# Optimization experiments

Hardware: AMD Instinct MI355X
Metric: run time of the kernel (lower is better)

Reference implementation:

```python
import jax, jax.numpy as jnp
import numpy as np

B, N, D, E = 256, 192, 512, 1024
H = E // 2          # MLP hidden = 512
K = 58              # round(0.3 * 192), hardcoded in the torch forward
EPS_L2 = 1e-8
EPS_BN = 1e-5


def setup_inputs() -> dict:
    key = jax.random.key(0)
    ks = jax.random.split(key, 8)
    s = 0.02
    return {
        "all_patch_embeddings": jax.random.normal(ks[0], (B, N, D), dtype=jnp.float32),
        "attention_map": jax.random.uniform(ks[1], (B, N + 1, N + 1), dtype=jnp.float32),
        # fc: Linear(D, E)
        "W_fc": jax.random.normal(ks[2], (E, D), dtype=jnp.float32) * s,
        "b_fc": jnp.zeros((E,), dtype=jnp.float32),
        # mlp layer 0: Linear(D, H) + BatchNorm1d(H) + ReLU
        "W1": jax.random.normal(ks[3], (H, D), dtype=jnp.float32) * s,
        "b1": jnp.zeros((H,), dtype=jnp.float32),
        "gamma1": jnp.ones((H,), dtype=jnp.float32),
        "beta1": jnp.zeros((H,), dtype=jnp.float32),
        # mlp layer 1: Linear(H, E) (no BN/ReLU applied on last layer)
        "W2": jax.random.normal(ks[4], (E, H), dtype=jnp.float32) * s,
        "b2": jnp.zeros((E,), dtype=jnp.float32),
    }


def reference(all_patch_embeddings, attention_map, W_fc, b_fc, W1, b1, gamma1, beta1, W2, b2):
    # CLS-row attention over the 192 patch tokens: [B, N]
    cls_attn = attention_map[:, 0, 1:]
    # torch.sort(descending)[...,:K] == top-k indices (batched, replaces python loop)
    _, idx = jax.lax.top_k(cls_attn, K)                      # [B, K] int32
    # batched gather replacing the per-sample index_select loop
    sel = jnp.take_along_axis(all_patch_embeddings, idx[:, :, None], axis=1)  # [B, K, D]
    # l2norm over last dim
    norm = jnp.sqrt(jnp.sum(sel * sel, axis=-1, keepdims=True)) + EPS_L2
    base = sel / norm
    # .half() cast in the original (round-trip to fp16 precision)
    base = base.astype(jnp.float16).astype(jnp.float32)
    # fc branch
    feat_fc = jnp.einsum('bkd,ed->bke', base, W_fc) + b_fc    # [B, K, E]
    # mlp branch (num_layers=2): Linear -> BN(train-mode batch stats) -> ReLU -> Linear
    h = jnp.einsum('bkd,hd->bkh', base, W1) + b1              # [B, K, H]
    hf = h.reshape(B * K, H)
    mu = jnp.mean(hf, axis=0)
    var = jnp.var(hf, axis=0)
    hf = (hf - mu) * jax.lax.rsqrt(var + EPS_BN) * gamma1 + beta1
    h = jax.nn.relu(hf).reshape(B, K, H)
    feat_mlp = jnp.einsum('bkh,eh->bke', h, W2) + b2          # [B, K, E]
    feats = feat_mlp + feat_fc
    # maxk_pool1d_var with k=1 and lengths == K reduces to max over token dim
    return jnp.max(feats, axis=1).astype(jnp.float32)         # [B, E]
```

## Files before the change

### kernel.cpp

```cpp
#include <hip/hip_runtime.h>
#include <hip/hip_fp16.h>

#define B_ 256
#define N_ 192
#define D_ 512
#define E_ 1024
#define H_ 512
#define K_ 58
#define M_ (B_*K_)
#define M2_ (B_*64)

typedef _Float16 f16;
typedef unsigned int u32;
typedef _Float16 half8 __attribute__((ext_vector_type(8)));
typedef float floatx16 __attribute__((ext_vector_type(16)));

#define WAIT_VMCNT0() asm volatile("s_waitcnt vmcnt(0)" ::: "memory")
#define BAR()         __builtin_amdgcn_s_barrier()
#define PRIO1()       __builtin_amdgcn_s_setprio(1)
#define PRIO0()       __builtin_amdgcn_s_setprio(0)

__device__ inline half8 cvt8(float4 f0, float4 f1) {
  half8 r;
  r[0]=(f16)f0.x; r[1]=(f16)f0.y; r[2]=(f16)f0.z; r[3]=(f16)f0.w;
  r[4]=(f16)f1.x; r[5]=(f16)f1.y; r[6]=(f16)f1.z; r[7]=(f16)f1.w;
  return r;
}

__device__ inline void gl_lds16(const f16* g, f16* l) {
  __builtin_amdgcn_global_load_lds((const __attribute__((address_space(1))) u32*)g,
                                   (__attribute__((address_space(3))) u32*)l, 16, 0, 0);
}

__device__ inline void stage128(const f16* gbase, int gstride, f16* sT, int w, int lane) {
  int lrow  = lane >> 2;
  int chunk = (lane & 3) ^ ((lane >> 3) & 3);
  gl_lds16(gbase + (size_t)(w*16      + lrow)*gstride + chunk*8, &sT[(w*16)*32]);
  gl_lds16(gbase + (size_t)(64 + w*16 + lrow)*gstride + chunk*8, &sT[(64 + w*16)*32]);
}

__device__ inline void stage_half(const f16* gbase, f16* sT, int h, int w, int lane) {
  int lrow = lane >> 3;
  int cg   = (lane & 7) ^ lrow;
  int r0 = h*128 + w*16;
  gl_lds16(gbase + (size_t)(r0     + lrow)*1024 + cg*8, &sT[(size_t)r0*64]);
  gl_lds16(gbase + (size_t)(r0 + 8 + lrow)*1024 + cg*8, &sT[(size_t)(r0 + 8)*64]);
}

__global__ void setup_kernel(const float* __restrict__ Wfc, const float* __restrict__ W2,
                             const float* __restrict__ W1, const float* __restrict__ attn,
                             const float* __restrict__ emb,
                             f16* __restrict__ Wcat, f16* __restrict__ W1_16,
                             f16* __restrict__ A16, float* __restrict__ csum) {
  __shared__ float sv[N_];
  __shared__ int sidx[K_];
  __shared__ int cnt;
  int blk = blockIdx.x, t = threadIdx.x;
  if (blk < 512) {
    int idx = (blk*256 + t)*8;
    int e = idx >> 10, c = idx & 1023;
    const float* src = (c < 512) ? (Wfc + (size_t)e*512 + c)
                                 : (W2  + (size_t)e*512 + (c-512));
    half8 o = cvt8(((const float4*)src)[0], ((const float4*)src)[1]);
    *(uint4*)(Wcat + idx) = *(uint4*)&o;
  } else if (blk < 640) {
    int idx = ((blk-512)*256 + t)*8;
    const float* src = W1 + idx;
    half8 o = cvt8(((const float4*)src)[0], ((const float4*)src)[1]);
    *(uint4*)(W1_16 + idx) = *(uint4*)&o;
  } else if (blk < 896) {
    int b = blk - 640;
    if (t == 0) cnt = 0;
    if (t < N_) sv[t] = attn[(size_t)b*193*193 + 1 + t];
    __syncthreads();
    if (t < N_) {
      float v = sv[t]; int rank = 0;
      for (int j = 0; j < N_; ++j) {
        float vj = sv[j];
        rank += (vj > v) || (vj == v && j < t);
      }
      if (rank < K_) sidx[atomicAdd(&cnt, 1)] = t;
    }
    __syncthreads();
    int w = t >> 6, lane = t & 63;
    for (int slot = w; slot < 64; slot += 4) {
      f16* dst = A16 + ((size_t)b*64 + slot)*1024 + lane*8;
      if (slot < K_) {
        const float* src = emb + ((size_t)b*N_ + sidx[slot])*D_ + lane*8;
        float4 v0 = ((const float4*)src)[0];
        float4 v1 = ((const float4*)src)[1];
        float s = v0.x*v0.x + v0.y*v0.y + v0.z*v0.z + v0.w*v0.w
                + v1.x*v1.x + v1.y*v1.y + v1.z*v1.z + v1.w*v1.w;
        #pragma unroll
        for (int off = 32; off > 0; off >>= 1) s += __shfl_xor(s, off);
        float inv = 1.0f / (sqrtf(s) + 1e-8f);
        half8 o;
        o[0]=(f16)(v0.x*inv); o[1]=(f16)(v0.y*inv); o[2]=(f16)(v0.z*inv); o[3]=(f16)(v0.w*inv);
        o[4]=(f16)(v1.x*inv); o[5]=(f16)(v1.y*inv); o[6]=(f16)(v1.z*inv); o[7]=(f16)(v1.w*inv);
        *(uint4*)dst = *(uint4*)&o;
      } else {
        uint4 z; z.x=0u; z.y=0u; z.z=0u; z.w=0u;
        *(uint4*)dst = z;
      }
    }
  } else {
    float4 z; z.x=0.f; z.y=0.f; z.z=0.f; z.w=0.f;
    ((float4*)csum)[t] = z;
  }
}

__launch_bounds__(256, 2)
__global__ void gemm1_kernel(const f16* __restrict__ A16, const f16* __restrict__ W1_16,
                             const float* __restrict__ b1, f16* __restrict__ Aout,
                             float* __restrict__ csum, float* __restrict__ css) {
  __shared__ f16 sA[2][128*32];
  __shared__ f16 sB[2][128*32];
  __shared__ float sSum[4][64], sSS[4][64];
  int t = threadIdx.x;
  int g = blockIdx.x;
  int xcd = g & 7, rest = g >> 3;
  int n0 = (rest & 3) * 128;
  int m0 = (xcd + 8*(rest >> 2)) * 128;
  int lane = t & 63, w = t >> 6;
  int l31 = lane & 31, khalf = lane >> 5, swz = (l31 >> 1) & 3;
  int rw = w & 1, cw = w >> 1;
  floatx16 acc[2][2] = {};
  const f16* Ab = A16 + (size_t)m0*1024;
  const f16* Bb = W1_16 + (size_t)n0*512;
  stage128(Ab, 1024, sA[0], w, lane);
  stage128(Bb, 512,  sB[0], w, lane);
  __syncthreads();
  for (int it = 0; it < 16; ++it) {
    int cur = it & 1, nxt = cur ^ 1;
    if (it < 15) {
      stage128(Ab + (it+1)*32, 1024, sA[nxt], w, lane);
      stage128(Bb + (it+1)*32, 512,  sB[nxt], w, lane);
    }
    #pragma unroll
    for (int s = 0; s < 2; ++s) {
      int ko = ((s*2 + khalf) ^ swz) * 8;
      half8 a[2], bf[2];
      #pragma unroll
      for (int i = 0; i < 2; ++i) a[i]  = *(const half8*)&sA[cur][(rw*64 + i*32 + l31)*32 + ko];
      #pragma unroll
      for (int j = 0; j < 2; ++j) bf[j] = *(const half8*)&sB[cur][(cw*64 + j*32 + l31)*32 + ko];
      #pragma unroll
      for (int i = 0; i < 2; ++i)
        #pragma unroll
        for (int j = 0; j < 2; ++j)
          acc[i][j] = __builtin_amdgcn_mfma_f32_32x32x16_f16(a[i], bf[j], acc[i][j], 0, 0, 0);
    }
    __syncthreads();
  }
  #pragma unroll
  for (int jt = 0; jt < 2; ++jt) {
    int col = n0 + cw*64 + jt*32 + l31;
    float bias = b1[col];
    float s = 0.f, ss = 0.f;
    #pragma unroll
    for (int i = 0; i < 2; ++i) {
      #pragma unroll
      for (int rg = 0; rg < 16; ++rg) {
        int rib = i*32 + (rg&3) + 8*(rg>>2) + 4*khalf;
        float x = acc[i][jt][rg] + bias;
        Aout[(size_t)(m0 + rw*64 + rib)*1024 + 512 + col] = (f16)x;
        if (i == 0 || rib < K_) { s += x; ss += x*x; }
      }
    }
    s  += __shfl_xor(s, 32);
    ss += __shfl_xor(ss, 32);
    if (lane < 32) { sSum[w][jt*32 + l31] = s; sSS[w][jt*32 + l31] = ss; }
  }
  __syncthreads();
  if (t < 128) {
    int c = t;
    int w0 = 2*(c >> 6), ci = c & 63;
    atomicAdd(&csum[n0 + c], sSum[w0][ci] + sSum[w0+1][ci]);
    atomicAdd(&css[n0 + c],  sSS[w0][ci]  + sSS[w0+1][ci]);
  }
}

__global__ void bnrelu_kernel(f16* __restrict__ A, const float* __restrict__ csum,
                              const float* __restrict__ css, const float* __restrict__ gamma,
                              const float* __restrict__ beta) {
  int t = threadIdx.x, lane = t & 63, w = t >> 6;
  int col = lane * 8;
  float sc[8], sh[8];
  #pragma unroll
  for (int j = 0; j < 8; ++j) {
    int c = col + j;
    float mu  = csum[c] * (1.0f/M_);
    float var = css[c] * (1.0f/M_) - mu*mu;
    float s   = gamma[c] * rsqrtf(var + 1e-5f);
    sc[j] = s; sh[j] = beta[c] - mu*s;
  }
  int r0 = blockIdx.x * 16 + w;
  #pragma unroll
  for (int i = 0; i < 4; ++i) {
    f16* p = A + (size_t)(r0 + i*4)*1024 + 512 + col;
    uint4 u = *(const uint4*)p;
    half8 v = *(half8*)&u, o;
    #pragma unroll
    for (int j = 0; j < 8; ++j) o[j] = (f16)fmaxf((float)v[j]*sc[j] + sh[j], 0.f);
    *(uint4*)p = *(uint4*)&o;
  }
}

__launch_bounds__(512, 2)
__global__ void fused_kernel(const f16* __restrict__ A16, const f16* __restrict__ Wcat,
                             const float* __restrict__ bfc, const float* __restrict__ b2,
                             float* __restrict__ out) {
  __shared__ __align__(16) f16 sA[2][256*64];
  __shared__ __align__(16) f16 sB[2][256*64];
  __shared__ float sMax[4][256];
  int t = threadIdx.x;
  int g = blockIdx.x;
  int xcd = g & 7, rest = g >> 3;
  int nt = rest & 3;
  int bt = xcd + 8*(rest >> 2);
  int e0 = nt * 256;
  int lane = t & 63, w = t >> 6;
  int l31 = lane & 31, khalf = lane >> 5, swzr = l31 & 7;
  int wm = w >> 2, wn = w & 3;
  floatx16 acc[4][2] = {};
  const f16* Ab = A16 + (size_t)bt*256*1024;
  const f16* Bb = Wcat + (size_t)e0*1024;
  int aBase0 = (wm*128 +  0 + l31)*64;
  int aBase1 = (wm*128 + 32 + l31)*64;
  int aBase2 = (wm*128 + 64 + l31)*64;
  int aBase3 = (wm*128 + 96 + l31)*64;
  int bBase0 = (wn*64  +  0 + l31)*64;
  int bBase1 = (wn*64  + 32 + l31)*64;
  stage_half(Ab, sA[0], 0, w, lane);
  stage_half(Ab, sA[0], 1, w, lane);
  stage_half(Bb, sB[0], 0, w, lane);
  stage_half(Bb, sB[0], 1, w, lane);
  WAIT_VMCNT0(); BAR();
  int cur = 0;
  #pragma unroll 1
  for (int it = 0; it < 16; ++it) {
    int nxt = cur ^ 1;
    const f16* An = Ab + (it+1)*64;
    const f16* Bn = Bb + (it+1)*64;
    const f16* sAc = sA[cur];
    const f16* sBc = sB[cur];
    half8 a0f[4], a1f[4], a2f[4], a3f[4], b0v[4], b1v[4];
    #pragma unroll
    for (int s = 0; s < 4; ++s) {
      int ko = (((s<<1)|khalf) ^ swzr) << 3;
      a0f[s] = *(const half8*)&sAc[aBase0 + ko];
      a1f[s] = *(const half8*)&sAc[aBase1 + ko];
      b0v[s] = *(const half8*)&sBc[bBase0 + ko];
    }
    if (it < 15) stage_half(An, sA[nxt], 0, w, lane);
    BAR(); PRIO1();
    #pragma unroll
    for (int s = 0; s < 4; ++s) {
      acc[0][0] = __builtin_amdgcn_mfma_f32_32x32x16_f16(a0f[s], b0v[s], acc[0][0], 0,0,0);
      acc[1][0] = __builtin_amdgcn_mfma_f32_32x32x16_f16(a1f[s], b0v[s], acc[1][0], 0,0,0);
    }
    PRIO0(); BAR();
    #pragma unroll
    for (int s = 0; s < 4; ++s) {
      int ko = (((s<<1)|khalf) ^ swzr) << 3;
      b1v[s] = *(const half8*)&sBc[bBase1 + ko];
    }
    if (it < 15) {
      stage_half(An, sA[nxt], 1, w, lane);
      stage_half(Bn, sB[nxt], 0, w, lane);
    }
    BAR(); PRIO1();
    #pragma unroll
    for (int s = 0; s < 4; ++s) {
      acc[0][1] = __builtin_amdgcn_mfma_f32_32x32x16_f16(a0f[s], b1v[s], acc[0][1], 0,0,0);
      acc[1][1] = __builtin_amdgcn_mfma_f32_32x32x16_f16(a1f[s], b1v[s], acc[1][1], 0,0,0);
    }
    PRIO0(); BAR();
    #pragma unroll
    for (int s = 0; s < 4; ++s) {
      int ko = (((s<<1)|khalf) ^ swzr) << 3;
      a2f[s] = *(const half8*)&sAc[aBase2 + ko];
      a3f[s] = *(const half8*)&sAc[aBase3 + ko];
    }
    if (it < 15) stage_half(Bn, sB[nxt], 1, w, lane);
    BAR(); PRIO1();
    #pragma unroll
    for (int s = 0; s < 4; ++s) {
      acc[2][1] = __builtin_amdgcn_mfma_f32_32x32x16_f16(a2f[s], b1v[s], acc[2][1], 0,0,0);
      acc[3][1] = __builtin_amdgcn_mfma_f32_32x32x16_f16(a3f[s], b1v[s], acc[3][1], 0,0,0);
    }
    PRIO0(); BAR();
    BAR(); PRIO1();
    #pragma unroll
    for (int s = 0; s < 4; ++s) {
      acc[2][0] = __builtin_amdgcn_mfma_f32_32x32x16_f16(a2f[s], b0v[s], acc[2][0], 0,0,0);
      acc[3][0] = __builtin_amdgcn_mfma_f32_32x32x16_f16(a3f[s], b0v[s], acc[3][0], 0,0,0);
    }
    PRIO0();
    WAIT_VMCNT0();
    BAR();
    cur = nxt;
  }
  #pragma unroll
  for (int p = 0; p < 2; ++p) {
    #pragma unroll
    for (int nf = 0; nf < 2; ++nf) {
      float mx = -3.0e38f;
      #pragma unroll
      for (int rg = 0; rg < 16; ++rg)
        mx = fmaxf(mx, acc[2*p][nf][rg]);
      #pragma unroll
      for (int rg = 0; rg < 16; ++rg) {
        int rowin = (rg&3) + 8*(rg>>2) + 4*khalf;
        if (rowin < K_ - 32) mx = fmaxf(mx, acc[2*p+1][nf][rg]);
      }
      mx = fmaxf(mx, __shfl_xor(mx, 32));
      if (lane < 32) sMax[wm*2 + p][wn*64 + nf*32 + l31] = mx;
    }
  }
  __syncthreads();
  #pragma unroll
  for (int j = 0; j < 2; ++j) {
    int idx = t + j*512;
    int bq = idx >> 8, c = idx & 255;
    int e = e0 + c;
    out[((size_t)bt*4 + bq)*E_ + e] = sMax[bq][c] + bfc[e] + b2[e];
  }
}

extern "C" void kernel_launch(void* const* d_in, const int* in_sizes, int n_in,
                              void* d_out, int out_size, void* d_ws, size_t ws_size,
                              hipStream_t stream) {
  const float* emb   = (const float*)d_in[0];
  const float* attn  = (const float*)d_in[1];
  const float* Wfc   = (const float*)d_in[2];
  const float* bfc   = (const float*)d_in[3];
  const float* W1    = (const float*)d_in[4];
  const float* b1    = (const float*)d_in[5];
  const float* gamma = (const float*)d_in[6];
  const float* beta  = (const float*)d_in[7];
  const float* W2    = (const float*)d_in[8];
  const float* b2    = (const float*)d_in[9];
  float* out = (float*)d_out;

  char* ws = (char*)d_ws;
  f16*   A16   = (f16*)(ws);
  f16*   Wcat  = (f16*)(ws + 33554432);
  f16*   W1_16 = (f16*)(ws + 35651584);
  float* csum  = (float*)(ws + 36175872);
  float* css   = (float*)(ws + 36177920);

  setup_kernel<<<897, 256, 0, stream>>>(Wfc, W2, W1, attn, emb, Wcat, W1_16, A16, csum);
  gemm1_kernel<<<512, 256, 0, stream>>>(A16, W1_16, b1, A16, csum, css);
  bnrelu_kernel<<<1024, 256, 0, stream>>>(A16, csum, css, gamma, beta);
  fused_kernel<<<256, 512, 0, stream>>>(A16, Wcat, bfc, b2, out);
}
```

Measured before the change: 235.2 us.

## Fuse BatchNorm+ReLU into final GEMM's A-tile staging, drop bnrelu kernel

Removes the separate bnrelu kernel. The fused GEMM now computes per-column scale and shift from the accumulated sums into shared memory. For the K-iterations covering the hidden half of A (iterations 7-14), it loads A through registers instead of global_load_lds, applies BN+ReLU, and writes the result into the swizzled LDS tile. This saves one kernel launch and a full read/write pass over the 16 MB hidden activation. In exchange, half of the A staging becomes synchronous register loads plus extra VALU work inside the main loop, which may reduce overlap.

```diff
diff --git a/kernel.cpp b/kernel.cpp
--- a/kernel.cpp
+++ b/kernel.cpp
@@ -16,6 +16,7 @@
 typedef float floatx16 __attribute__((ext_vector_type(16)));
 
 #define WAIT_VMCNT0() asm volatile("s_waitcnt vmcnt(0)" ::: "memory")
+#define WAIT_LGKM0()  asm volatile("s_waitcnt lgkmcnt(0)" ::: "memory")
 #define BAR()         __builtin_amdgcn_s_barrier()
 #define PRIO1()       __builtin_amdgcn_s_setprio(1)
 #define PRIO0()       __builtin_amdgcn_s_setprio(0)
@@ -25,6 +26,19 @@
   r[0]=(f16)f0.x; r[1]=(f16)f0.y; r[2]=(f16)f0.z; r[3]=(f16)f0.w;
   r[4]=(f16)f1.x; r[5]=(f16)f1.y; r[6]=(f16)f1.z; r[7]=(f16)f1.w;
   return r;
+}
+
+__device__ inline uint4 bn8(uint4 u, float4 sc0, float4 sc1, float4 sh0, float4 sh1) {
+  half8 v = *(half8*)&u, o;
+  o[0]=(f16)fmaxf((float)v[0]*sc0.x+sh0.x, 0.f);
+  o[1]=(f16)fmaxf((float)v[1]*sc0.y+sh0.y, 0.f);
+  o[2]=(f16)fmaxf((float)v[2]*sc0.z+sh0.z, 0.f);
+  o[3]=(f16)fmaxf((float)v[3]*sc0.w+sh0.w, 0.f);
+  o[4]=(f16)fmaxf((float)v[4]*sc1.x+sh1.x, 0.f);
+  o[5]=(f16)fmaxf((float)v[5]*sc1.y+sh1.y, 0.f);
+  o[6]=(f16)fmaxf((float)v[6]*sc1.z+sh1.z, 0.f);
+  o[7]=(f16)fmaxf((float)v[7]*sc1.w+sh1.w, 0.f);
+  return *(uint4*)&o;
 }
 
 __device__ inline void gl_lds16(const f16* g, f16* l) {
@@ -180,39 +194,16 @@
   }
 }
 
-__global__ void bnrelu_kernel(f16* __restrict__ A, const float* __restrict__ csum,
-                              const float* __restrict__ css, const float* __restrict__ gamma,
-                              const float* __restrict__ beta) {
-  int t = threadIdx.x, lane = t & 63, w = t >> 6;
-  int col = lane * 8;
-  float sc[8], sh[8];
-  #pragma unroll
-  for (int j = 0; j < 8; ++j) {
-    int c = col + j;
-    float mu  = csum[c] * (1.0f/M_);
-    float var = css[c] * (1.0f/M_) - mu*mu;
-    float s   = gamma[c] * rsqrtf(var + 1e-5f);
-    sc[j] = s; sh[j] = beta[c] - mu*s;
-  }
-  int r0 = blockIdx.x * 16 + w;
-  #pragma unroll
-  for (int i = 0; i < 4; ++i) {
-    f16* p = A + (size_t)(r0 + i*4)*1024 + 512 + col;
-    uint4 u = *(const uint4*)p;
-    half8 v = *(half8*)&u, o;
-    #pragma unroll
-    for (int j = 0; j < 8; ++j) o[j] = (f16)fmaxf((float)v[j]*sc[j] + sh[j], 0.f);
-    *(uint4*)p = *(uint4*)&o;
-  }
-}
-
 __launch_bounds__(512, 2)
 __global__ void fused_kernel(const f16* __restrict__ A16, const f16* __restrict__ Wcat,
+                             const float* __restrict__ csum, const float* __restrict__ css,
+                             const float* __restrict__ gamma, const float* __restrict__ beta,
                              const float* __restrict__ bfc, const float* __restrict__ b2,
                              float* __restrict__ out) {
   __shared__ __align__(16) f16 sA[2][256*64];
   __shared__ __align__(16) f16 sB[2][256*64];
   __shared__ float sMax[4][256];
+  __shared__ float sSc[H_], sSh[H_];
   int t = threadIdx.x;
   int g = blockIdx.x;
   int xcd = g & 7, rest = g >> 3;
@@ -222,6 +213,7 @@
   int lane = t & 63, w = t >> 6;
   int l31 = lane & 31, khalf = lane >> 5, swzr = l31 & 7;
   int wm = w >> 2, wn = w & 3;
+  int lrow = lane >> 3, cg = (lane & 7) ^ lrow;
   floatx16 acc[4][2] = {};
   const f16* Ab = A16 + (size_t)bt*256*1024;
   const f16* Bb = Wcat + (size_t)e0*1024;
@@ -235,7 +227,15 @@
   stage_half(Ab, sA[0], 1, w, lane);
   stage_half(Bb, sB[0], 0, w, lane);
   stage_half(Bb, sB[0], 1, w, lane);
-  WAIT_VMCNT0(); BAR();
+  {
+    int c = t;
+    float mu  = csum[c] * (1.0f/M_);
+    float var = css[c] * (1.0f/M_) - mu*mu;
+    float sc  = gamma[c] * rsqrtf(var + 1e-5f);
+    sSc[c] = sc;
+    sSh[c] = beta[c] - mu*sc;
+  }
+  WAIT_VMCNT0(); WAIT_LGKM0(); BAR();
   int cur = 0;
   #pragma unroll 1
   for (int it = 0; it < 16; ++it) {
@@ -244,6 +244,8 @@
     const f16* Bn = Bb + (it+1)*64;
     const f16* sAc = sA[cur];
     const f16* sBc = sB[cur];
+    bool rp = (it >= 7) && (it < 15);
+    uint4 ra0, ra1, ra2, ra3;
     half8 a0f[4], a1f[4], a2f[4], a3f[4], b0v[4], b1v[4];
     #pragma unroll
     for (int s = 0; s < 4; ++s) {
@@ -252,7 +254,14 @@
       a1f[s] = *(const half8*)&sAc[aBase1 + ko];
       b0v[s] = *(const half8*)&sBc[bBase0 + ko];
     }
-    if (it < 15) stage_half(An, sA[nxt], 0, w, lane);
+    if (it < 15) {
+      if (!rp) stage_half(An, sA[nxt], 0, w, lane);
+      else {
+        const f16* gp = An + (size_t)(w*16 + lrow)*1024 + cg*8;
+        ra0 = *(const uint4*)gp;
+        ra1 = *(const uint4*)(gp + (size_t)8*1024);
+      }
+    }
     BAR(); PRIO1();
     #pragma unroll
     for (int s = 0; s < 4; ++s) {
@@ -266,7 +275,12 @@
       b1v[s] = *(const half8*)&sBc[bBase1 + ko];
     }
     if (it < 15) {
-      stage_half(An, sA[nxt], 1, w, lane);
+      if (!rp) stage_half(An, sA[nxt], 1, w, lane);
+      else {
+        const f16* gp = An + (size_t)(128 + w*16 + lrow)*1024 + cg*8;
+        ra2 = *(const uint4*)gp;
+        ra3 = *(const uint4*)(gp + (size_t)8*1024);
+      }
       stage_half(Bn, sB[nxt], 0, w, lane);
     }
     BAR(); PRIO1();
@@ -297,6 +311,17 @@
       acc[3][0] = __builtin_amdgcn_mfma_f32_32x32x16_f16(a3f[s], b0v[s], acc[3][0], 0,0,0);
     }
     PRIO0();
+    if (rp) {
+      int c = (it + 1)*64 - 512 + cg*8;
+      float4 sc0 = *(float4*)&sSc[c], sc1 = *(float4*)&sSc[c+4];
+      float4 sh0 = *(float4*)&sSh[c], sh1 = *(float4*)&sSh[c+4];
+      int r0 = w*16 + lrow, sl = (lane & 7)*8;
+      *(uint4*)&sA[nxt][(r0      )*64 + sl] = bn8(ra0, sc0, sc1, sh0, sh1);
+      *(uint4*)&sA[nxt][(r0 +   8)*64 + sl] = bn8(ra1, sc0, sc1, sh0, sh1);
+      *(uint4*)&sA[nxt][(r0 + 128)*64 + sl] = bn8(ra2, sc0, sc1, sh0, sh1);
+      *(uint4*)&sA[nxt][(r0 + 136)*64 + sl] = bn8(ra3, sc0, sc1, sh0, sh1);
+      WAIT_LGKM0();
+    }
     WAIT_VMCNT0();
     BAR();
     cur = nxt;
@@ -352,6 +377,5 @@
 
   setup_kernel<<<897, 256, 0, stream>>>(Wfc, W2, W1, attn, emb, Wcat, W1_16, A16, csum);
   gemm1_kernel<<<512, 256, 0, stream>>>(A16, W1_16, b1, A16, csum, css);
-  bnrelu_kernel<<<1024, 256, 0, stream>>>(A16, csum, css, gamma, beta);
-  fused_kernel<<<256, 512, 0, stream>>>(A16, Wcat, bfc, b2, out);
-}
+  fused_kernel<<<256, 512, 0, stream>>>(A16, Wcat, csum, css, gamma, beta, bfc, b2, out);
+}
```

Result: no change. 238.1 us (+1.2%).
